# Optimization experiments

Measured on AMD Instinct MI355X. Metric: run time of the kernel, lower is better.

The kernel has to match this reference:

```python
import jax, jax.numpy as jnp
import numpy as np

N_QUBITS = 10      # = hidden_dim; state vector has 2**10 = 1024 amplitudes
T, B, D = 128, 256, 64
H = N_QUBITS
DIM = 2 ** N_QUBITS


def _rx(theta):
    # RX(t) = [[cos(t/2), -i sin(t/2)], [-i sin(t/2), cos(t/2)]]; theta scalar or (B,)
    c = jnp.cos(theta / 2).astype(jnp.complex64)
    s = (-1j) * jnp.sin(theta / 2).astype(jnp.complex64)
    return jnp.stack([jnp.stack([c, s], -1), jnp.stack([s, c], -1)], -2)


def _ry(theta):
    c = jnp.cos(theta / 2)
    s = jnp.sin(theta / 2)
    return jnp.stack([jnp.stack([c, -s], -1), jnp.stack([s, c], -1)], -2).astype(jnp.complex64)


def _rz(theta):
    em = jnp.exp(-0.5j * theta.astype(jnp.complex64))
    ep = jnp.exp(0.5j * theta.astype(jnp.complex64))
    z = jnp.zeros_like(em)
    return jnp.stack([jnp.stack([em, z], -1), jnp.stack([z, ep], -1)], -2)


def _apply_1q(state, mat, w):
    # state: (B, 2^n) complex; wire 0 is the most-significant axis (torchquantum layout)
    b = state.shape[0]
    s = state.reshape(b, 2 ** w, 2, -1)
    if mat.ndim == 2:
        out = jnp.einsum('ij,bljr->blir', mat, s)
    else:  # batched encoding angles: mat (B,2,2)
        out = jnp.einsum('bij,bljr->blir', mat, s)
    return out.reshape(b, -1)


def _apply_cnot(state, a, bq):
    # control a < target bq: flip target axis in the control=1 block
    b = state.shape[0]
    s = state.reshape(b, 2 ** a, 2, 2 ** (bq - a - 1), 2, -1)
    new = jnp.stack([s[:, :, 0], s[:, :, 1, :, ::-1]], axis=2)
    return new.reshape(b, -1)


def qgate(x, params):
    # x: (B, n) classical features -> PauliZ expectations per wire (B, n)
    n = N_QUBITS
    b = x.shape[0]
    state = jnp.zeros((b, 2 ** n), jnp.complex64).at[:, 0].set(1.0 + 0.0j)
    for w in range(n):                       # RX encoding of input features
        state = _apply_1q(state, _rx(x[:, w]), w)
    for w in range(n):                       # parameterized RX, RY, RZ per wire
        state = _apply_1q(state, _rx(params[w, 0]), w)
        state = _apply_1q(state, _ry(params[w, 1]), w)
        state = _apply_1q(state, _rz(params[w, 2]), w)
    for a in range(n - 1):                   # CNOT chain entanglement
        state = _apply_cnot(state, a, a + 1)
    probs = jnp.real(state * jnp.conj(state))
    zs = []
    for w in range(n):                       # <Z_w> = P(bit_w=0) - P(bit_w=1)
        p = probs.reshape(b, 2 ** w, 2, -1)
        zs.append(p[:, :, 0, :].sum((1, 2)) - p[:, :, 1, :].sum((1, 2)))
    return jnp.stack(zs, axis=1)


def setup_inputs() -> dict:
    key = jax.random.key(0)
    ks = jax.random.split(key, 16)
    scale = 1.0 / np.sqrt(D + H)
    inp = {'inputs': jax.random.normal(ks[0], (T, B, D), jnp.float32)}
    for i, g in enumerate(['f', 'i', 'u', 'o']):
        inp['W' + g] = jax.random.normal(ks[1 + 3 * i], (H, D + H), jnp.float32) * scale
        inp['b' + g] = jax.random.normal(ks[2 + 3 * i], (H,), jnp.float32) * scale
        inp['p' + g] = jax.random.normal(ks[3 + 3 * i], (H, 3), jnp.float32)
    inp['ln_g'] = jnp.ones((H,), jnp.float32)
    inp['ln_b'] = jnp.zeros((H,), jnp.float32)
    return inp


def reference(inputs, Wf, bf, pf, Wi, bi, pi, Wu, bu, pu, Wo, bo, po, ln_g, ln_b):
    b = inputs.shape[1]

    def step(carry, x):
        hx, cx = carry
        comb = jnp.concatenate([x, hx], axis=1)
        f = jax.nn.sigmoid(qgate(comb @ Wf.T + bf, pf))
        i = jax.nn.sigmoid(qgate(comb @ Wi.T + bi, pi))
        g = jnp.tanh(qgate(comb @ Wu.T + bu, pu))
        o = jax.nn.sigmoid(qgate(comb @ Wo.T + bo, po))
        cx2 = f * cx + i * g
        h = o * jnp.tanh(cx2) + hx  # residual skip
        mu = h.mean(-1, keepdims=True)
        var = ((h - mu) ** 2).mean(-1, keepdims=True)
        h = (h - mu) / jnp.sqrt(var + 1e-5) * ln_g + ln_b  # LayerNorm
        # dropout: identity in eval mode
        return (h, cx2), h

    init = (jnp.zeros((b, H), jnp.float32), jnp.zeros((b, H), jnp.float32))
    (hx, cx), ys = jax.lax.scan(step, init, inputs)
    return ys, hx, cx
```

## Files before the change

### kernel.cpp

```cpp
#include <hip/hip_runtime.h>
#include <hip/hip_bf16.h>
#include <math.h>


#define T_STEPS 128
#define B_SZ    256
#define D_IN    64
#define H_SZ    10
#define COMB    74

template<int CTRL>
__device__ __forceinline__ float dpp_mov(float old_, float src) {
    return __int_as_float(__builtin_amdgcn_update_dpp(
        __float_as_int(old_), __float_as_int(src), CTRL, 0xF, 0xF, false));
}
#define DPP_ROW_SHR(n) (0x110 + (n))
#define DPP_ROW_ROR(n) (0x120 + (n))

__device__ __forceinline__ float rdlane(float v, int lane) {
    return __int_as_float(__builtin_amdgcn_readlane(__float_as_int(v), lane));
}
__device__ __forceinline__ float bperm(int lane, float v) {
    return __int_as_float(__builtin_amdgcn_ds_bpermute(4 * lane, __float_as_int(v)));
}
__device__ __forceinline__ float frcp(float x) { return __builtin_amdgcn_rcpf(x); }

__device__ __forceinline__ float tanh_pade(float x) {
    float x2  = x * x;
    float num = x * fmaf(x2, (x2 + 105.f), 945.f);
    float den = fmaf(x2, fmaf(x2, 15.f, 420.f), 945.f);
    return num * frcp(den);
}

__global__ __launch_bounds__(64) void qlstm_pre(
    const float* __restrict__ x,
    const float* __restrict__ Wf, const float* __restrict__ bf,
    const float* __restrict__ Wi, const float* __restrict__ bi,
    const float* __restrict__ Wu, const float* __restrict__ bu,
    const float* __restrict__ Wo, const float* __restrict__ bo,
    float* __restrict__ Zx)
{
    __shared__ float Wl[40 * 64];
    __shared__ float bl[40];

    const int tid = threadIdx.x;
    const long r0 = (long)blockIdx.x * 128 + tid;
    const long r1 = r0 + 64;

    const float* Ws[4] = {Wf, Wi, Wu, Wo};
    const float* bs[4] = {bf, bi, bu, bo};
#pragma unroll
    for (int k = 0; k < 40; k++) {
        int gg = k / 10, w = k - gg * 10;
        Wl[k * 64 + tid] = Ws[gg][w * COMB + tid];
    }
    if (tid < 40) { int gg = tid / 10, w = tid - gg * 10; bl[tid] = bs[gg][w]; }
    __syncthreads();

    float xr0[64], xr1[64];
    const float4* xin0 = (const float4*)(x + r0 * D_IN);
    const float4* xin1 = (const float4*)(x + r1 * D_IN);
#pragma unroll
    for (int k = 0; k < 16; k++) {
        float4 v0 = xin0[k];
        xr0[4*k+0] = v0.x; xr0[4*k+1] = v0.y; xr0[4*k+2] = v0.z; xr0[4*k+3] = v0.w;
        float4 v1 = xin1[k];
        xr1[4*k+0] = v1.x; xr1[4*k+1] = v1.y; xr1[4*k+2] = v1.z; xr1[4*k+3] = v1.w;
    }

    const int t0 = (int)(r0 >> 8), b0 = (int)(r0 & 255);
    const int t1 = (int)(r1 >> 8), b1 = (int)(r1 & 255);
    float* z0 = Zx + (size_t)b0 * 40 * T_STEPS + t0;
    float* z1 = Zx + (size_t)b1 * 40 * T_STEPS + t1;

#pragma unroll
    for (int gw = 0; gw < 40; gw++) {
        float a0 = bl[gw], a1 = bl[gw];
        const float4* wr4 = (const float4*)(Wl + gw * 64);
#pragma unroll
        for (int d4 = 0; d4 < 16; d4++) {
            float4 wv = wr4[d4];
            a0 = fmaf(xr0[4*d4+0], wv.x, a0);
            a0 = fmaf(xr0[4*d4+1], wv.y, a0);
            a0 = fmaf(xr0[4*d4+2], wv.z, a0);
            a0 = fmaf(xr0[4*d4+3], wv.w, a0);
            a1 = fmaf(xr1[4*d4+0], wv.x, a1);
            a1 = fmaf(xr1[4*d4+1], wv.y, a1);
            a1 = fmaf(xr1[4*d4+2], wv.z, a1);
            a1 = fmaf(xr1[4*d4+3], wv.w, a1);
        }
        z0[(size_t)gw * T_STEPS] = a0;
        z1[(size_t)gw * T_STEPS] = a1;
    }
}

__global__ __launch_bounds__(64) void qlstm_rec(
    const float* __restrict__ Zx,
    const float* __restrict__ Wf, const float* __restrict__ Wi,
    const float* __restrict__ Wu, const float* __restrict__ Wo,
    const float* __restrict__ pf, const float* __restrict__ pi,
    const float* __restrict__ pu, const float* __restrict__ po,
    const float* __restrict__ ln_g, const float* __restrict__ ln_b,
    float* __restrict__ ys, float* __restrict__ outH, float* __restrict__ outC)
{
    const int b    = blockIdx.x;
    const int lane = threadIdx.x;
    const int g    = lane >> 4;
    const int w    = lane & 15;
    const bool act = (w < H_SZ);

    const float* Ws[4] = {Wf, Wi, Wu, Wo};
    const float* ps[4] = {pf, pi, pu, po};

    float whp[H_SZ];
    float S = 0.f, A = 0.f;
#pragma unroll
    for (int j = 0; j < H_SZ; j++) {
        float whj = act ? Ws[g][w * COMB + D_IN + j] : 0.f;
        whp[j] = whj * ln_g[j];
        S += whp[j];
        A  = fmaf(whj, ln_b[j], A);
    }
    const float p0  = act ? ps[g][w * 3 + 0] : 0.f;
    const float cp1 = act ? __cosf(ps[g][w * 3 + 1]) : 1.f;
    const float lng = act ? ln_g[w] : 0.f;
    const float lnb = act ? ln_b[w] : 0.f;
    const float s0 = (g == 2) ? 0.f : 0.5f;
    const float s1 = (g == 2) ? 1.f : 0.5f;
    const float sc = (g == 2) ? 1.f : 0.5f;

    float hn = 0.f;
    float cc = 0.f;
    float hterm = 0.f;

    const int gwl = g * 10 + (act ? w : 9);
    const float* zb = Zx + ((size_t)b * 40 + gwl) * T_STEPS;
    float4 zb0 = *(const float4*)(zb);
    float4 zb1 = *(const float4*)(zb + 4);

    float* ysb = ys + (size_t)b * H_SZ + lane;

    for (int gq = 0; gq < T_STEPS / 4; gq++) {
        float4 zc = zb0;
        zb0 = zb1;
        const int nl = (gq + 2 < T_STEPS / 4) ? gq + 2 : T_STEPS / 4 - 1;
        zb1 = *(const float4*)(zb + (size_t)nl * 4);

        float zs[4] = {zc.x, zc.y, zc.z, zc.w};
#pragma unroll
        for (int j = 0; j < 4; j++) {
            const int t = gq * 4 + j;
            float z = zs[j] + hterm;

            float prod = cp1 * __cosf(p0 + z);
            prod *= dpp_mov<DPP_ROW_SHR(1)>(1.f, prod);
            prod *= dpp_mov<DPP_ROW_SHR(2)>(1.f, prod);
            prod *= dpp_mov<DPP_ROW_SHR(4)>(1.f, prod);
            prod *= dpp_mov<DPP_ROW_SHR(8)>(1.f, prod);

            float av = fmaf(s1, tanh_pade(sc * prod), s0);

            float fw = bperm(w,      av);
            float iw = bperm(w + 16, av);
            float uw = bperm(w + 32, av);
            float ow = bperm(w + 48, av);

            cc = fmaf(fw, cc, iw * uw);
            float tc   = tanh_pade(cc);
            float hraw = fmaf(ow, tc, hn);

            float v1 = act ? hraw : 0.f;
            float v2 = v1 * v1;
            v1 += dpp_mov<DPP_ROW_ROR(8)>(0.f, v1);
            v2 += dpp_mov<DPP_ROW_ROR(8)>(0.f, v2);
            v1 += dpp_mov<DPP_ROW_ROR(4)>(0.f, v1);
            v2 += dpp_mov<DPP_ROW_ROR(4)>(0.f, v2);
            v1 += dpp_mov<DPP_ROW_ROR(2)>(0.f, v1);
            v2 += dpp_mov<DPP_ROW_ROR(2)>(0.f, v2);
            v1 += dpp_mov<DPP_ROW_ROR(1)>(0.f, v1);
            v2 += dpp_mov<DPP_ROW_ROR(1)>(0.f, v2);

            float d0 = whp[0] * rdlane(hraw, 0);
            float d1 = whp[1] * rdlane(hraw, 1);
            d0 = fmaf(whp[2], rdlane(hraw, 2), d0);
            d1 = fmaf(whp[3], rdlane(hraw, 3), d1);
            d0 = fmaf(whp[4], rdlane(hraw, 4), d0);
            d1 = fmaf(whp[5], rdlane(hraw, 5), d1);
            d0 = fmaf(whp[6], rdlane(hraw, 6), d0);
            d1 = fmaf(whp[7], rdlane(hraw, 7), d1);
            d0 = fmaf(whp[8], rdlane(hraw, 8), d0);
            d1 = fmaf(whp[9], rdlane(hraw, 9), d1);
            float D = d0 + d1;

            float mu   = v1 * 0.1f;
            float varr = fmaxf(fmaf(v2, 0.1f, -mu * mu), 0.f);
            float rstd = __builtin_amdgcn_rsqf(varr + 1e-5f);

            hn    = fmaf((hraw - mu) * rstd, lng, lnb);
            hterm = fmaf(rstd, fmaf(-mu, S, D), A);

            if (lane < H_SZ)
                ysb[(size_t)t * B_SZ * H_SZ] = hn;
        }
    }

    if (lane < H_SZ) {
        outH[b * H_SZ + lane] = hn;
        outC[b * H_SZ + lane] = cc;
    }
}

extern "C" void kernel_launch(void* const* d_in, const int* in_sizes, int n_in,
                              void* d_out, int out_size, void* d_ws, size_t ws_size,
                              hipStream_t stream)
{
    const float* x    = (const float*)d_in[0];
    const float* Wf   = (const float*)d_in[1];
    const float* bf   = (const float*)d_in[2];
    const float* pf   = (const float*)d_in[3];
    const float* Wi   = (const float*)d_in[4];
    const float* bi   = (const float*)d_in[5];
    const float* pi   = (const float*)d_in[6];
    const float* Wu   = (const float*)d_in[7];
    const float* bu   = (const float*)d_in[8];
    const float* pu   = (const float*)d_in[9];
    const float* Wo   = (const float*)d_in[10];
    const float* bo   = (const float*)d_in[11];
    const float* po   = (const float*)d_in[12];
    const float* ln_g = (const float*)d_in[13];
    const float* ln_b = (const float*)d_in[14];

    float* Zx = (float*)d_ws;

    float* ys   = (float*)d_out;
    float* outH = ys + (size_t)T_STEPS * B_SZ * H_SZ;
    float* outC = outH + (size_t)B_SZ * H_SZ;

    qlstm_pre<<<(T_STEPS * B_SZ) / 128, 64, 0, stream>>>(
        x, Wf, bf, Wi, bi, Wu, bu, Wo, bo, Zx);

    qlstm_rec<<<B_SZ, 64, 0, stream>>>(
        Zx, Wf, Wi, Wu, Wo, pf, pi, pu, po, ln_g, ln_b, ys, outH, outC);
}
```

Before: 141.2 us.

## Fuse input projection into recurrent kernel via shared-memory Z buffer

Merges the input-projection kernel and the recurrence kernel into one launch. Each block, one per batch element, has 128 threads compute the 40 gate pre-activations for all 128 timesteps into padded shared memory, and then one wavefront runs the sequential recurrence reading from LDS. This removes the global workspace round trip and a kernel launch. The cost is that the projection now runs redundantly per block with weights reloaded, and the block holds about 31KB of LDS.

```diff
diff --git a/kernel.cpp b/kernel.cpp
--- a/kernel.cpp
+++ b/kernel.cpp
@@ -1,5 +1,4 @@
 #include <hip/hip_runtime.h>
-#include <hip/hip_bf16.h>
 #include <math.h>
 
 
@@ -8,6 +7,7 @@
 #define D_IN    64
 #define H_SZ    10
 #define COMB    74
+#define ZPAD    132
 
 template<int CTRL>
 __device__ __forceinline__ float dpp_mov(float old_, float src) {
@@ -32,79 +32,72 @@
     return num * frcp(den);
 }
 
-__global__ __launch_bounds__(64) void qlstm_pre(
+__global__ __launch_bounds__(128) void qlstm_fused(
     const float* __restrict__ x,
-    const float* __restrict__ Wf, const float* __restrict__ bf,
-    const float* __restrict__ Wi, const float* __restrict__ bi,
-    const float* __restrict__ Wu, const float* __restrict__ bu,
-    const float* __restrict__ Wo, const float* __restrict__ bo,
-    float* __restrict__ Zx)
-{
-    __shared__ float Wl[40 * 64];
-    __shared__ float bl[40];
-
-    const int tid = threadIdx.x;
-    const long r0 = (long)blockIdx.x * 128 + tid;
-    const long r1 = r0 + 64;
-
-    const float* Ws[4] = {Wf, Wi, Wu, Wo};
-    const float* bs[4] = {bf, bi, bu, bo};
-#pragma unroll
-    for (int k = 0; k < 40; k++) {
-        int gg = k / 10, w = k - gg * 10;
-        Wl[k * 64 + tid] = Ws[gg][w * COMB + tid];
-    }
-    if (tid < 40) { int gg = tid / 10, w = tid - gg * 10; bl[tid] = bs[gg][w]; }
-    __syncthreads();
-
-    float xr0[64], xr1[64];
-    const float4* xin0 = (const float4*)(x + r0 * D_IN);
-    const float4* xin1 = (const float4*)(x + r1 * D_IN);
-#pragma unroll
-    for (int k = 0; k < 16; k++) {
-        float4 v0 = xin0[k];
-        xr0[4*k+0] = v0.x; xr0[4*k+1] = v0.y; xr0[4*k+2] = v0.z; xr0[4*k+3] = v0.w;
-        float4 v1 = xin1[k];
-        xr1[4*k+0] = v1.x; xr1[4*k+1] = v1.y; xr1[4*k+2] = v1.z; xr1[4*k+3] = v1.w;
-    }
-
-    const int t0 = (int)(r0 >> 8), b0 = (int)(r0 & 255);
-    const int t1 = (int)(r1 >> 8), b1 = (int)(r1 & 255);
-    float* z0 = Zx + (size_t)b0 * 40 * T_STEPS + t0;
-    float* z1 = Zx + (size_t)b1 * 40 * T_STEPS + t1;
-
-#pragma unroll
-    for (int gw = 0; gw < 40; gw++) {
-        float a0 = bl[gw], a1 = bl[gw];
-        const float4* wr4 = (const float4*)(Wl + gw * 64);
-#pragma unroll
-        for (int d4 = 0; d4 < 16; d4++) {
-            float4 wv = wr4[d4];
-            a0 = fmaf(xr0[4*d4+0], wv.x, a0);
-            a0 = fmaf(xr0[4*d4+1], wv.y, a0);
-            a0 = fmaf(xr0[4*d4+2], wv.z, a0);
-            a0 = fmaf(xr0[4*d4+3], wv.w, a0);
-            a1 = fmaf(xr1[4*d4+0], wv.x, a1);
-            a1 = fmaf(xr1[4*d4+1], wv.y, a1);
-            a1 = fmaf(xr1[4*d4+2], wv.z, a1);
-            a1 = fmaf(xr1[4*d4+3], wv.w, a1);
-        }
-        z0[(size_t)gw * T_STEPS] = a0;
-        z1[(size_t)gw * T_STEPS] = a1;
-    }
-}
-
-__global__ __launch_bounds__(64) void qlstm_rec(
-    const float* __restrict__ Zx,
-    const float* __restrict__ Wf, const float* __restrict__ Wi,
-    const float* __restrict__ Wu, const float* __restrict__ Wo,
-    const float* __restrict__ pf, const float* __restrict__ pi,
-    const float* __restrict__ pu, const float* __restrict__ po,
+    const float* __restrict__ Wf, const float* __restrict__ bf, const float* __restrict__ pf,
+    const float* __restrict__ Wi, const float* __restrict__ bi, const float* __restrict__ pi,
+    const float* __restrict__ Wu, const float* __restrict__ bu, const float* __restrict__ pu,
+    const float* __restrict__ Wo, const float* __restrict__ bo, const float* __restrict__ po,
     const float* __restrict__ ln_g, const float* __restrict__ ln_b,
     float* __restrict__ ys, float* __restrict__ outH, float* __restrict__ outC)
 {
-    const int b    = blockIdx.x;
-    const int lane = threadIdx.x;
+    __shared__ __align__(16) float Wl[40 * 64];
+    __shared__ __align__(16) float Zl[40 * ZPAD];
+    __shared__ float bl[40];
+
+    const int tid = threadIdx.x;
+    const int b   = blockIdx.x;
+
+    float xr[64];
+    const float4* xin = (const float4*)(x + ((size_t)tid * B_SZ + b) * D_IN);
+#pragma unroll
+    for (int k = 0; k < 16; k++) {
+        float4 v = xin[k];
+        xr[4*k+0] = v.x; xr[4*k+1] = v.y; xr[4*k+2] = v.z; xr[4*k+3] = v.w;
+    }
+
+#pragma unroll
+    for (int k = 0; k < 20; k++) {
+        int idx = k * 128 + tid;
+        int r   = idx >> 6;
+        int col = idx & 63;
+        const float* Wp; int w;
+        if      (r < 10) { Wp = Wf; w = r;      }
+        else if (r < 20) { Wp = Wi; w = r - 10; }
+        else if (r < 30) { Wp = Wu; w = r - 20; }
+        else             { Wp = Wo; w = r - 30; }
+        Wl[idx] = Wp[w * COMB + col];
+    }
+    if (tid < 40) {
+        int r = tid;
+        const float* bp; int w;
+        if      (r < 10) { bp = bf; w = r;      }
+        else if (r < 20) { bp = bi; w = r - 10; }
+        else if (r < 30) { bp = bu; w = r - 20; }
+        else             { bp = bo; w = r - 30; }
+        bl[tid] = bp[w];
+    }
+    __syncthreads();
+
+#pragma unroll
+    for (int gw = 0; gw < 40; gw++) {
+        float a = bl[gw];
+        const float4* wr4 = (const float4*)(Wl + gw * 64);
+#pragma unroll
+        for (int d4 = 0; d4 < 16; d4++) {
+            float4 wv = wr4[d4];
+            a = fmaf(xr[4*d4+0], wv.x, a);
+            a = fmaf(xr[4*d4+1], wv.y, a);
+            a = fmaf(xr[4*d4+2], wv.z, a);
+            a = fmaf(xr[4*d4+3], wv.w, a);
+        }
+        Zl[gw * ZPAD + tid] = a;
+    }
+    __syncthreads();
+
+    if (tid >= 64) return;
+
+    const int lane = tid;
     const int g    = lane >> 4;
     const int w    = lane & 15;
     const bool act = (w < H_SZ);
@@ -134,7 +127,7 @@
     float hterm = 0.f;
 
     const int gwl = g * 10 + (act ? w : 9);
-    const float* zb = Zx + ((size_t)b * 40 + gwl) * T_STEPS;
+    const float* zb = Zl + (size_t)gwl * ZPAD;
     float4 zb0 = *(const float4*)(zb);
     float4 zb1 = *(const float4*)(zb + 4);
 
@@ -230,15 +223,11 @@
     const float* ln_g = (const float*)d_in[13];
     const float* ln_b = (const float*)d_in[14];
 
-    float* Zx = (float*)d_ws;
-
     float* ys   = (float*)d_out;
     float* outH = ys + (size_t)T_STEPS * B_SZ * H_SZ;
     float* outC = outH + (size_t)B_SZ * H_SZ;
 
-    qlstm_pre<<<(T_STEPS * B_SZ) / 128, 64, 0, stream>>>(
-        x, Wf, bf, Wi, bi, Wu, bu, Wo, bo, Zx);
-
-    qlstm_rec<<<B_SZ, 64, 0, stream>>>(
-        Zx, Wf, Wi, Wu, Wo, pf, pi, pu, po, ln_g, ln_b, ys, outH, outC);
-}
+    qlstm_fused<<<B_SZ, 128, 0, stream>>>(
+        x, Wf, bf, pf, Wi, bi, pi, Wu, bu, pu, Wo, bo, po,
+        ln_g, ln_b, ys, outH, outC);
+}
```

Result: faster. 128.8 us (-8.8%).
